# Kernel optimization log

Hardware: AMD Instinct MI355X
Metric: run time of the kernel (lower is better)

## Reference

```python
import jax, jax.numpy as jnp
import numpy as np

B, P, M, N, H, K, EH = 16, 50, 512, 1024, 64, 20, 200


def setup_inputs() -> dict:
    key = jax.random.key(0)
    ks = jax.random.split(key, 16)
    b = jax.random.normal(ks[0], (B, P, M, 1), jnp.float32)
    A = jax.random.normal(ks[1], (1, P, M, N), jnp.float32) / np.float32(np.sqrt(M))
    # random undirected multigraph on P nodes, stored with both directions
    s = jax.random.randint(ks[2], (B, EH), 0, P)
    off = jax.random.randint(ks[3], (B, EH), 1, P)
    d = (s + off) % P
    edge_index = jnp.stack([jnp.concatenate([s, d], 1), jnp.concatenate([d, s], 1)], 1).astype(jnp.int32)  # [B,2,2*EH]

    def lin(k, fi, fo, scale=None):
        scale = np.float32(1.0 / np.sqrt(fi)) if scale is None else np.float32(scale)
        return jax.random.normal(k, (fi, fo), jnp.float32) * scale, jnp.zeros((fo,), jnp.float32)

    W_e1, b_e1 = lin(ks[4], P * M, P * H)
    W_e2, b_e2 = lin(ks[5], P * H, 2 * P * H)
    W_e3, b_e3 = lin(ks[6], 2 * P * H, 4 * P * H)
    W_c1, b_c1 = lin(ks[7], 4 * H, 2 * H)
    W_c2, b_c2 = lin(ks[8], 2 * H, 2 * H)
    W_f1, b_f1 = lin(ks[9], 2 * H, H)
    W_f2, _ = lin(ks[10], H, K * 4, scale=1e-3)
    b_f2 = jnp.full((K * 4,), -2.0, jnp.float32)  # mimics fc2 init (tiny weights, negative bias)
    max_param = jnp.array([0.01, 0.1, 0.1, 0.1], jnp.float32).reshape(1, 1, 1, 4)  # [alpha,tau,rho,eta]_max
    y0 = jax.random.normal(ks[11], (B, P, N, 1), jnp.float32) * 0.01
    u0 = jax.random.normal(ks[12], (B, P, N, 1), jnp.float32) * 0.01
    d0 = jax.random.normal(ks[13], (B, P, N, 1), jnp.float32) * 0.01
    return dict(b=b, A=A, edge_index=edge_index, max_param=max_param,
                W_e1=W_e1, b_e1=b_e1, W_e2=W_e2, b_e2=b_e2, W_e3=W_e3, b_e3=b_e3,
                W_c1=W_c1, b_c1=b_c1, W_c2=W_c2, b_c2=b_c2,
                W_f1=W_f1, b_f1=b_f1, W_f2=W_f2, b_f2=b_f2,
                y0=y0, u0=u0, d0=d0)


def _lrelu(x):
    return jax.nn.leaky_relu(x, 0.01)


def _gcn(x, s, d, W, bias):
    # GCNConv: sym-normalized propagation with self loops. x: [P,F]
    h = x @ W
    deg = jnp.zeros((x.shape[0],), x.dtype).at[d].add(1.0) + 1.0  # +1 self loop
    dinv = jax.lax.rsqrt(deg)
    agg = jnp.zeros_like(h).at[d].add(h[s] * (dinv[s] * dinv[d])[:, None])
    agg = agg + h * (dinv * dinv)[:, None]  # self-loop term
    return agg + bias


def _delta(y, s, d):
    # nested neighbor loop: for each directed edge (s,d): delta[s]+=y[s]-y[d]; delta[d]-=same
    diff = y[s] - y[d]  # [E,N,1]
    return jnp.zeros_like(y).at[s].add(diff).at[d].add(-diff)


def reference(b, A, edge_index, max_param,
              W_e1, b_e1, W_e2, b_e2, W_e3, b_e3,
              W_c1, b_c1, W_c2, b_c2, W_f1, b_f1, W_f2, b_f2,
              y0, u0, d0):
    Bb = b.shape[0]
    n = A.shape[3]
    k_steps = W_f2.shape[1] // 4
    src, dst = edge_index[:, 0], edge_index[:, 1]

    # ---- GNN hypernetwork ----
    x = b.reshape(Bb, -1)
    x = _lrelu(x @ W_e1 + b_e1)
    x = _lrelu(x @ W_e2 + b_e2)
    x = (x @ W_e3 + b_e3).reshape(Bb, P, -1)  # [B,P,4H]
    x = _lrelu(jax.vmap(lambda xf, s, d: _gcn(xf, s, d, W_c1, b_c1))(x, src, dst))
    x = _lrelu(jax.vmap(lambda xf, s, d: _gcn(xf, s, d, W_c2, b_c2))(x, src, dst))
    x = x.mean(axis=1)  # global_mean_pool over nodes
    x = _lrelu(x @ W_f1 + b_f1)
    hyp = (x @ W_f2 + b_f2).reshape(Bb, k_steps, 1, 4)
    hyp = jax.nn.sigmoid(jnp.cumsum(hyp, axis=1)) * max_param  # [B,K,1,4]
    hyp_scan = jnp.transpose(hyp, (1, 3, 0, 2))[..., None, None]  # [K,4,B,1,1,1]

    # ---- precompute ----
    A0 = A[0]  # [P,M,N]
    AtA = jnp.einsum('pmn,pmk->pnk', A0, A0)  # [P,N,N]
    Atb = jnp.einsum('pmn,bpmo->bpno', A0, b)  # [B,P,N,1]
    sum_nb = jax.vmap(lambda s: jnp.zeros((P,), b.dtype).at[s].add(1.0))(src)[:, :, None, None]  # [B,P,1,1]

    # ---- unrolled D-ADMM / DLASSO ----
    def step(carry, hk):
        y_k, U_k, dlt = carry
        alpha, tau, rho, eta = hk[0], hk[1], hk[2], hk[3]
        AtAy = jnp.einsum('pnk,bpko->bpno', AtA, y_k)
        g = AtAy - Atb + jnp.sign(y_k) * tau + U_k * sum_nb + dlt * rho
        y_n = y_k - alpha * g
        dlt_n = jax.vmap(_delta)(y_n, src, dst)
        U_n = U_k + dlt_n * eta
        return (y_n, U_n, dlt_n), y_n

    _, Y = jax.lax.scan(step, (y0, u0, d0), hyp_scan)
    return Y  # [K,B,P,N,1]
```

## Files before the change

### kernel.cpp

```cpp
#include <hip/hip_runtime.h>

namespace {
constexpr int NB = 16;
constexpr int NP = 50;
constexpr int NM = 512;
constexpr int NN = 1024;
constexpr int NK = 20;
constexpr long ASZ = (long)NP * NM * NN;
constexpr long YSZ = (long)NB * NP * NN;
}

typedef __attribute__((ext_vector_type(8))) short bf16x8;
typedef __attribute__((ext_vector_type(4))) float f32x4;

__device__ __forceinline__ float lrelu(float x){ return x > 0.f ? x : 0.01f*x; }
__device__ __forceinline__ float bfu(unsigned short x){
  unsigned v = ((unsigned)x) << 16;
  return __builtin_bit_cast(float, v);
}
__device__ __forceinline__ unsigned short f2bf(float f){
  unsigned u = __builtin_bit_cast(unsigned, f);
  u += 0x7fffu + ((u >> 16) & 1u);
  return (unsigned short)(u >> 16);
}
__device__ __forceinline__ long toff(int n, int kk){
  return (long)(n>>4)*16384 + (long)(kk>>5)*512 + (long)((n&15)*32 + ((kk>>3)&3)*8 + (kk&7));
}

__global__ __launch_bounds__(256) void k_prep(const float* __restrict__ A,
                      unsigned short* __restrict__ abfT){
  const int p = blockIdx.x, mt = blockIdx.y, nt = blockIdx.z;
  const int tid = threadIdx.x;
  __shared__ unsigned short tile[64][72];
  const int m0 = mt*64, n0 = nt*64;
  {
    int r = tid>>2, cs = (tid&3)*16;
    const float* src = A + ((long)p*NM + m0 + r)*NN + n0 + cs;
    unsigned short tmp[16];
    #pragma unroll
    for (int q=0;q<16;q+=4){
      float4 v = *(const float4*)(src+q);
      tmp[q+0]=f2bf(v.x); tmp[q+1]=f2bf(v.y); tmp[q+2]=f2bf(v.z); tmp[q+3]=f2bf(v.w);
    }
    #pragma unroll
    for (int q=0;q<16;q++) tile[r][cs+q] = tmp[q];
  }
  __syncthreads();
  {
    int r = tid>>2, cs = (tid&3)*16;
    unsigned short* dst = abfT + ((long)p*NN + n0 + r)*NM + m0 + cs;
    unsigned short tmp[16];
    #pragma unroll
    for (int q=0;q<16;q++) tmp[q] = tile[cs+q][r];
    #pragma unroll
    for (int q=0;q<16;q+=8) *(uint4*)(dst+q) = *(const uint4*)&tmp[q];
  }
}

__global__ void k_init(const float* __restrict__ y0, float* __restrict__ y,
                       unsigned short* __restrict__ ybf, int n){
  int e = (blockIdx.x*blockDim.x + threadIdx.x)*4;
  if (e >= n) return;
  float4 a = *(const float4*)(y0+e);
  *(float4*)(y+e) = a;
  ushort4 o; o.x=f2bf(a.x); o.y=f2bf(a.y); o.z=f2bf(a.z); o.w=f2bf(a.w);
  *(ushort4*)(ybf+e) = o;
}

__global__ __launch_bounds__(256) void k_e0(const float* __restrict__ u0,
      const float* __restrict__ d0, const float* __restrict__ atb,
      const float* __restrict__ snbg, const float* __restrict__ hypg,
      float* __restrict__ w, float* __restrict__ e){
  long i = ((long)blockIdx.x*256 + threadIdx.x)*4;
  if (i >= YSZ) return;
  long bp = i >> 10;
  int b = (int)(bp/NP), p = (int)(bp%NP);
  float sp = snbg[b*NP+p], rho = hypg[b*80 + 2];
  float4 uv = *(const float4*)(u0+i);
  float4 dv = *(const float4*)(d0+i);
  float4 av = *(const float4*)(atb+i);
  float4 wv, ev;
  wv.x = uv.x*sp - av.x; wv.y = uv.y*sp - av.y;
  wv.z = uv.z*sp - av.z; wv.w = uv.w*sp - av.w;
  ev.x = wv.x + dv.x*rho; ev.y = wv.y + dv.y*rho;
  ev.z = wv.z + dv.z*rho; ev.w = wv.w + dv.w*rho;
  *(float4*)(w+i) = wv;
  *(float4*)(e+i) = ev;
}


__device__ __forceinline__ void enc_body(const float* __restrict__ X, const float* __restrict__ W,
                           float* __restrict__ part, int fi, int fo, int ichunk, int actin,
                           int bx, int c, int tid, char* smem){
  float (*xs)[16] = (float(*)[16])smem;
  const int o0 = (bx*256 + tid)*4;
  const bool ok = o0 < fo;
  float4 acc[16];
  #pragma unroll
  for (int b=0;b<16;b++){ acc[b].x=0.f; acc[b].y=0.f; acc[b].z=0.f; acc[b].w=0.f; }
  const long ibase = (long)c*ichunk;
  const int xb = tid&15, xio = (tid>>4)*4;
  for (int s=0; s<ichunk; s+=64){
    float4 v = *(const float4*)(X + (long)xb*fi + ibase + s + xio);
    if (actin){ v.x=lrelu(v.x); v.y=lrelu(v.y); v.z=lrelu(v.z); v.w=lrelu(v.w); }
    __syncthreads();
    xs[xio+0][xb]=v.x; xs[xio+1][xb]=v.y; xs[xio+2][xb]=v.z; xs[xio+3][xb]=v.w;
    __syncthreads();
    const float* wp = W + (ibase+s)*fo + o0;
    #pragma unroll 4
    for (int i=0;i<64;i++){
      float4 w;
      if (ok) w = *(const float4*)(wp + (long)i*fo);
      else { w.x=0.f; w.y=0.f; w.z=0.f; w.w=0.f; }
      #pragma unroll
      for (int b2=0;b2<16;b2+=4){
        float4 x4 = *(const float4*)&xs[i][b2];
        acc[b2+0].x += w.x*x4.x; acc[b2+0].y += w.y*x4.x; acc[b2+0].z += w.z*x4.x; acc[b2+0].w += w.w*x4.x;
        acc[b2+1].x += w.x*x4.y; acc[b2+1].y += w.y*x4.y; acc[b2+1].z += w.z*x4.y; acc[b2+1].w += w.w*x4.y;
        acc[b2+2].x += w.x*x4.z; acc[b2+2].y += w.y*x4.z; acc[b2+2].z += w.z*x4.z; acc[b2+2].w += w.w*x4.z;
        acc[b2+3].x += w.x*x4.w; acc[b2+3].y += w.y*x4.w; acc[b2+3].z += w.z*x4.w; acc[b2+3].w += w.w*x4.w;
      }
    }
  }
  if (ok){
    float* pp = part + ((long)c*16)*fo + o0;
    #pragma unroll
    for (int b=0;b<16;b++) *(float4*)(pp + (long)b*fo) = acc[b];
  }
}

__device__ __forceinline__ void ata_body(const unsigned short* __restrict__ abfT,
                      unsigned short* __restrict__ ata, int yy_in, int p, int tid, char* smem){
  unsigned short (*pa)[72] = (unsigned short(*)[72])smem;
  unsigned short (*pb)[72] = (unsigned short(*)[72])(smem + 18432);
  int yy = yy_in, bi = 0;
  while (yy >= 8 - bi){ yy -= 8 - bi; bi++; }
  const int bj = bi + yy;
  const int i0 = bi*128, j0 = bj*128;
  const int wave = tid>>6, lane = tid&63;
  const int lr = lane&15, kg = lane>>4;
  f32x4 acc[2][8];
  #pragma unroll
  for (int ti=0;ti<2;ti++)
    #pragma unroll
    for (int tj=0;tj<8;tj++) acc[ti][tj] = (f32x4){0.f,0.f,0.f,0.f};
  const unsigned short* Abase = abfT + (long)p*NN*NM;
  for (int mc=0; mc<NM; mc+=64){
    __syncthreads();
    {
      int r = tid>>1, c0 = (tid&1)*32;
      const unsigned short* sa = Abase + (long)(i0 + r)*NM + mc + c0;
      const unsigned short* sb = Abase + (long)(j0 + r)*NM + mc + c0;
      #pragma unroll
      for (int q=0;q<32;q+=8){
        *(uint4*)&pa[r][c0+q] = *(const uint4*)(sa+q);
        *(uint4*)&pb[r][c0+q] = *(const uint4*)(sb+q);
      }
    }
    __syncthreads();
    #pragma unroll
    for (int ks=0; ks<2; ks++){
      bf16x8 av0 = *(const bf16x8*)&pa[wave*32      + lr][ks*32 + kg*8];
      bf16x8 av1 = *(const bf16x8*)&pa[wave*32 + 16 + lr][ks*32 + kg*8];
      #pragma unroll
      for (int tj=0;tj<8;tj++){
        bf16x8 bv = *(const bf16x8*)&pb[tj*16 + lr][ks*32 + kg*8];
        acc[0][tj] = __builtin_amdgcn_mfma_f32_16x16x32_bf16(av0, bv, acc[0][tj], 0,0,0);
        acc[1][tj] = __builtin_amdgcn_mfma_f32_16x16x32_bf16(av1, bv, acc[1][tj], 0,0,0);
      }
    }
  }
  const long pbase = (long)p << 20;
  #pragma unroll
  for (int ti=0; ti<2; ti++){
    const int ib = i0 + wave*32 + ti*16;
    #pragma unroll
    for (int tj=0; tj<8; tj++){
      const int jb = j0 + tj*16;
      unsigned short w[4];
      #pragma unroll
      for (int r=0;r<4;r++) w[r] = f2bf(acc[ti][tj][r]);
      #pragma unroll
      for (int r=0;r<4;r++)
        ata[pbase + toff(ib + kg*4 + r, jb + lr)] = w[r];
      if (bi != bj){
        #pragma unroll
        for (int r=0;r<4;r++)
          ata[pbase + toff(jb + lr, ib + kg*4 + r)] = w[r];
      }
    }
  }
}

__device__ __forceinline__ void atb_body(const unsigned short* __restrict__ abfT,
                      const float* __restrict__ src, float* __restrict__ z,
                      int p, int gy, int tid, char* smem){
  unsigned short (*tlds)[520] = (unsigned short(*)[520])smem;
  const int wave = tid>>6, lane = tid&63;
  {
    int b = tid>>4, c0 = (tid&15)*8;
    const float* tr = src + ((long)b*NP + p)*NM;
    #pragma unroll
    for (int it=0; it<4; it++){
      float4 lo = *(const float4*)(tr + it*128 + c0);
      float4 hi = *(const float4*)(tr + it*128 + c0 + 4);
      unsigned short w[8];
      w[0]=f2bf(lo.x); w[1]=f2bf(lo.y); w[2]=f2bf(lo.z); w[3]=f2bf(lo.w);
      w[4]=f2bf(hi.x); w[5]=f2bf(hi.y); w[6]=f2bf(hi.z); w[7]=f2bf(hi.w);
      *(uint4*)&tlds[b][it*128 + c0] = *(const uint4*)w;
    }
  }
  __syncthreads();
  const int lr = lane&15, kg = lane>>4;
  const int nt0 = gy*4 + wave;
  const int n0 = nt0*16, n1 = (nt0+32)*16;
  const unsigned short* b0 = abfT + ((long)p*NN + n0 + lr)*NM + kg*8;
  const unsigned short* b1 = abfT + ((long)p*NN + n1 + lr)*NM + kg*8;
  const unsigned short* tp = &tlds[lr][kg*8];
  f32x4 acc0a={0.f,0.f,0.f,0.f}, acc0b={0.f,0.f,0.f,0.f};
  f32x4 acc1a={0.f,0.f,0.f,0.f}, acc1b={0.f,0.f,0.f,0.f};
  #pragma unroll 4
  for (int ks=0; ks<16; ks+=2){
    bf16x8 t0 = *(const bf16x8*)(tp + ks*32);
    bf16x8 t1 = *(const bf16x8*)(tp + ks*32 + 32);
    bf16x8 b00 = *(const bf16x8*)(b0 + (long)ks*32);
    bf16x8 b01 = *(const bf16x8*)(b0 + (long)ks*32 + 32);
    bf16x8 b10 = *(const bf16x8*)(b1 + (long)ks*32);
    bf16x8 b11 = *(const bf16x8*)(b1 + (long)ks*32 + 32);
    acc0a = __builtin_amdgcn_mfma_f32_16x16x32_bf16(t0, b00, acc0a, 0, 0, 0);
    acc1a = __builtin_amdgcn_mfma_f32_16x16x32_bf16(t0, b10, acc1a, 0, 0, 0);
    acc0b = __builtin_amdgcn_mfma_f32_16x16x32_bf16(t1, b01, acc0b, 0, 0, 0);
    acc1b = __builtin_amdgcn_mfma_f32_16x16x32_bf16(t1, b11, acc1b, 0, 0, 0);
  }
  f32x4 acc0 = acc0a + acc0b;
  f32x4 acc1 = acc1a + acc1b;
  #pragma unroll
  for (int r=0;r<4;r++){
    int bb = kg*4 + r;
    z[((long)bb*NP + p)*NN + n0 + lr] = acc0[r];
    z[((long)bb*NP + p)*NN + n1 + lr] = acc1[r];
  }
}

__global__ __launch_bounds__(256) void k_big(const unsigned short* __restrict__ abfT,
      unsigned short* __restrict__ ata, const float* __restrict__ bin,
      const float* __restrict__ We1, float* __restrict__ part,
      float* __restrict__ atb){
  __shared__ __align__(16) char smem[36864];
  const int bid = blockIdx.x, tid = threadIdx.x;
  if (bid < 800){
    enc_body(bin, We1, part, 25600, 3200, 128, 0, bid & 3, bid >> 2, tid, smem);
  } else if (bid < 2600){
    int a = bid - 800;
    ata_body(abfT, ata, a % 36, a / 36, tid, smem);
  } else {
    int a = bid - 2600;
    atb_body(abfT, bin, atb, a >> 3, a & 7, tid, smem);
  }
}

__global__ __launch_bounds__(256) void k_enc2(const float* __restrict__ X, const float* __restrict__ W,
                           float* __restrict__ part, int fi, int fo, int ichunk, int actin){
  __shared__ __align__(16) char smem[4096];
  enc_body(X, W, part, fi, fo, ichunk, actin, blockIdx.x, blockIdx.y, threadIdx.x, smem);
}

__global__ void k_enc_reduce(const float* __restrict__ part, const float* __restrict__ bias,
                             float* __restrict__ out, int fo, int nchunk){
  int i = blockIdx.x*256 + threadIdx.x;
  if (i >= 16*fo) return;
  int o = i % fo;
  float s = bias[o];
  for (int c=0;c<nchunk;c++) s += part[(long)c*16*fo + i];
  out[i] = s;
}

__global__ __launch_bounds__(64) void k_graph(const int* __restrict__ ei, float* __restrict__ adjg,
                        float* __restrict__ dmg, float* __restrict__ snbg){
  const int b = blockIdx.x, tid = threadIdx.x;
  __shared__ float adj[2500], dm[2500], deg[50], dinv[50], snb[50];
  for (int i=tid;i<2500;i+=64){ adj[i]=0.f; dm[i]=0.f; }
  if (tid<50){ deg[tid]=0.f; snb[tid]=0.f; }
  __syncthreads();
  const int* e = ei + b*800;
  for (int k=tid;k<400;k+=64){
    atomicAdd(&deg[e[400+k]], 1.f);
    atomicAdd(&snb[e[k]], 1.f);
  }
  __syncthreads();
  if (tid<50) dinv[tid] = 1.f / sqrtf(deg[tid] + 1.f);
  __syncthreads();
  for (int k=tid;k<400;k+=64){
    int s = e[k], d = e[400+k];
    atomicAdd(&adj[d*50+s], dinv[s]*dinv[d]);
    atomicAdd(&dm[s*50+s],  1.f); atomicAdd(&dm[s*50+d], -1.f);
    atomicAdd(&dm[d*50+d],  1.f); atomicAdd(&dm[d*50+s], -1.f);
  }
  __syncthreads();
  if (tid<50) adj[tid*50+tid] += dinv[tid]*dinv[tid];
  __syncthreads();
  for (int i=tid;i<2500;i+=64){ adjg[b*2500+i]=adj[i]; dmg[b*2500+i]=dm[i]; }
  if (tid<50) snbg[b*50+tid]=snb[tid];
}

__global__ __launch_bounds__(256) void k_gnn(const float* __restrict__ h3,
     const float* __restrict__ Wc1, const float* __restrict__ bc1,
     const float* __restrict__ Wc2, const float* __restrict__ bc2,
     const float* __restrict__ Wf1, const float* __restrict__ bf1,
     const float* __restrict__ Wf2, const float* __restrict__ bf2,
     const float* __restrict__ maxp, const float* __restrict__ adjg,
     float* __restrict__ hypg){
  const int b = blockIdx.x, tid = threadIdx.x;
  __shared__ float adj[2500];
  __shared__ float bufA[6400];
  __shared__ float bufB[6400];
  __shared__ float xm[128], hv1[64], raw[80];
  for (int i=tid;i<2500;i+=256) adj[i] = adjg[b*2500+i];

  const int j = tid & 127, nh = tid >> 7;
  float acc[25];
  #pragma unroll
  for (int q=0;q<25;q++) acc[q]=0.f;
  for (int ic=0; ic<4; ic++){
    __syncthreads();
    for (int e=tid; e<800; e+=256){
      int n = e>>4, seg = (e&15)*4;
      *(float4*)&bufB[n*64+seg] = *(const float4*)(h3 + (long)b*12800 + n*256 + ic*64 + seg);
    }
    __syncthreads();
    for (int i=0;i<64;i+=4){
      float w0 = Wc1[(long)(ic*64+i+0)*128 + j];
      float w1 = Wc1[(long)(ic*64+i+1)*128 + j];
      float w2 = Wc1[(long)(ic*64+i+2)*128 + j];
      float w3 = Wc1[(long)(ic*64+i+3)*128 + j];
      #pragma unroll
      for (int q=0;q<25;q++){
        float4 xv = *(const float4*)&bufB[(nh*25+q)*64 + i];
        acc[q] += xv.x*w0 + xv.y*w1 + xv.z*w2 + xv.w*w3;
      }
    }
  }
  __syncthreads();
  #pragma unroll
  for (int q=0;q<25;q++) bufA[(nh*25+q)*128 + j] = acc[q];
  __syncthreads();
  {
    float a2[25];
    float bv = bc1[j];
    #pragma unroll
    for (int q=0;q<25;q++) a2[q]=bv;
    for (int qq=0; qq<50; qq++){
      float hvv = bufA[qq*128 + j];
      #pragma unroll
      for (int q=0;q<25;q++) a2[q] += adj[(nh*25+q)*50 + qq]*hvv;
    }
    __syncthreads();
    #pragma unroll
    for (int q=0;q<25;q++) bufB[(nh*25+q)*128 + j] = lrelu(a2[q]);
  }
  __syncthreads();
  {
    float a2[25];
    #pragma unroll
    for (int q=0;q<25;q++) a2[q]=0.f;
    for (int i=0;i<128;i+=4){
      float w0 = Wc2[(long)(i+0)*128 + j];
      float w1 = Wc2[(long)(i+1)*128 + j];
      float w2 = Wc2[(long)(i+2)*128 + j];
      float w3 = Wc2[(long)(i+3)*128 + j];
      #pragma unroll
      for (int q=0;q<25;q++){
        float4 xv = *(const float4*)&bufB[(nh*25+q)*128 + i];
        a2[q] += xv.x*w0 + xv.y*w1 + xv.z*w2 + xv.w*w3;
      }
    }
    __syncthreads();
    #pragma unroll
    for (int q=0;q<25;q++) bufA[(nh*25+q)*128 + j] = a2[q];
  }
  __syncthreads();
  {
    float a2[25];
    float bv = bc2[j];
    #pragma unroll
    for (int q=0;q<25;q++) a2[q]=bv;
    for (int qq=0; qq<50; qq++){
      float hvv = bufA[qq*128 + j];
      #pragma unroll
      for (int q=0;q<25;q++) a2[q] += adj[(nh*25+q)*50 + qq]*hvv;
    }
    __syncthreads();
    #pragma unroll
    for (int q=0;q<25;q++) bufB[(nh*25+q)*128 + j] = lrelu(a2[q]);
  }
  __syncthreads();
  if (tid < 128){
    float s = 0.f;
    for (int n=0;n<50;n++) s += bufB[n*128 + tid];
    xm[tid] = s * (1.f/50.f);
  }
  __syncthreads();
  if (tid < 64){
    float s = bf1[tid];
    for (int i=0;i<128;i++) s += xm[i]*Wf1[i*64 + tid];
    hv1[tid] = lrelu(s);
  }
  __syncthreads();
  if (tid < 80){
    float s = bf2[tid];
    for (int i=0;i<64;i++) s += hv1[i]*Wf2[i*80 + tid];
    raw[tid] = s;
  }
  __syncthreads();
  if (tid < 4){
    float c = 0.f;
    for (int k=0;k<20;k++){
      c += raw[k*4 + tid];
      hypg[b*80 + k*4 + tid] = maxp[tid] / (1.f + expf(-c));
    }
  }
}

__global__ __launch_bounds__(256, 4) void k_z(const unsigned short* __restrict__ ata,
      const unsigned short* __restrict__ ybin, const float* __restrict__ ebuf,
      const float* __restrict__ hypg, int k,
      float* __restrict__ y, unsigned short* __restrict__ ybout,
      float* __restrict__ yout){
  const int p = blockIdx.x;
  const int tid = threadIdx.x, wave = tid>>6, lane = tid&63;
  __shared__ unsigned short ylds[16][1032];
  {
    int b = tid>>4, c0 = (tid&15)*8;
    const unsigned short* yr = ybin + ((long)b*NP + p)*NN;
    #pragma unroll
    for (int it=0; it<8; it++)
      *(uint4*)&ylds[b][it*128 + c0] = *(const uint4*)(yr + it*128 + c0);
  }
  const int lr = lane&15, kg = lane>>4;
  const int t  = blockIdx.y*4 + wave;
  const int n0 = t*16;
  const unsigned short* bp = ata + ((long)p<<20) + (long)t*16384 + lr*32 + kg*8;
  const unsigned short* yp = &ylds[lr][kg*8];

  bf16x8 B[3][4];
  #pragma unroll
  for (int j=0;j<4;j++) B[0][j] = *(const bf16x8*)(bp + (0*4+j)*512);
  #pragma unroll
  for (int j=0;j<4;j++) B[1][j] = *(const bf16x8*)(bp + (1*4+j)*512);

  float yv4[4], e4[4];
  float4 hp4[4];
  #pragma unroll
  for (int r=0;r<4;r++){
    const int b = kg*4 + r;
    const long idx = ((long)b*NP + p)*NN + n0 + lr;
    yv4[r] = y[idx]; e4[r] = ebuf[idx];
    hp4[r] = *(const float4*)(hypg + b*80 + k*4);
  }
  __syncthreads();

  f32x4 a0={0.f,0.f,0.f,0.f}, a1={0.f,0.f,0.f,0.f}, a2={0.f,0.f,0.f,0.f}, a3={0.f,0.f,0.f,0.f};
  #pragma unroll
  for (int i=0;i<8;i++){
    const int cur = i % 3;
    const int nxt = (i+2) % 3;
    if (i < 6){
      #pragma unroll
      for (int j=0;j<4;j++) B[nxt][j] = *(const bf16x8*)(bp + ((i+2)*4+j)*512);
    }
    bf16x8 q0 = *(const bf16x8*)(yp + (i*4+0)*32);
    bf16x8 q1 = *(const bf16x8*)(yp + (i*4+1)*32);
    bf16x8 q2 = *(const bf16x8*)(yp + (i*4+2)*32);
    bf16x8 q3 = *(const bf16x8*)(yp + (i*4+3)*32);
    a0 = __builtin_amdgcn_mfma_f32_16x16x32_bf16(q0, B[cur][0], a0, 0,0,0);
    a1 = __builtin_amdgcn_mfma_f32_16x16x32_bf16(q1, B[cur][1], a1, 0,0,0);
    a2 = __builtin_amdgcn_mfma_f32_16x16x32_bf16(q2, B[cur][2], a2, 0,0,0);
    a3 = __builtin_amdgcn_mfma_f32_16x16x32_bf16(q3, B[cur][3], a3, 0,0,0);
  }
  f32x4 z = (a0 + a1) + (a2 + a3);
  #pragma unroll
  for (int r=0;r<4;r++){
    const int b = kg*4 + r;
    const long idx = ((long)b*NP + p)*NN + n0 + lr;
    float yv = yv4[r];
    float g = z[r] + ((yv>0.f)?1.f:((yv<0.f)?-1.f:0.f))*hp4[r].y + e4[r];
    float ynv = yv - hp4[r].x*g;
    y[idx] = ynv; ybout[idx] = f2bf(ynv); yout[(long)k*YSZ + idx] = ynv;
  }
}

__global__ __launch_bounds__(256) void k_dm(const float* __restrict__ dmg,
      const float* __restrict__ snbg, const float* __restrict__ hypg, int k,
      const unsigned short* __restrict__ ybf, float* __restrict__ w, float* __restrict__ e){
  const int b = blockIdx.x, n0 = blockIdx.y*64, tid = threadIdx.x;
  __shared__ float ys[50][64];
  __shared__ float dms[2500];
  for (int i=tid;i<2500;i+=256) dms[i] = dmg[b*2500+i];
  for (int i=tid; i<3200; i+=256){
    int p=i>>6, nn=i&63;
    ys[p][nn] = bfu(ybf[((long)b*NP+p)*NN + n0 + nn]);
  }
  __syncthreads();
  const float eta = hypg[b*80 + k*4 + 3];
  const float rhon = hypg[b*80 + (k+1)*4 + 2];
  for (int i=tid; i<3200; i+=256){
    int p=i>>6, nn=i&63;
    float s=0.f;
    #pragma unroll 10
    for (int q=0;q<NP;q++) s += dms[p*50+q]*ys[q][nn];
    long idx = ((long)b*NP+p)*NN + n0 + nn;
    float wn = w[idx] + s*eta*snbg[b*NP+p];
    w[idx] = wn;
    e[idx] = wn + s*rhon;
  }
}

extern "C" void kernel_launch(void* const* d_in, const int* in_sizes, int n_in,
                              void* d_out, int out_size, void* d_ws, size_t ws_size,
                              hipStream_t stream){
  (void)in_sizes; (void)n_in; (void)out_size; (void)ws_size;
  const float* bin = (const float*)d_in[0];
  const float* A   = (const float*)d_in[1];
  const int*   ei  = (const int*)d_in[2];
  const float* mxp = (const float*)d_in[3];
  const float* We1 = (const float*)d_in[4];  const float* be1 = (const float*)d_in[5];
  const float* We2 = (const float*)d_in[6];  const float* be2 = (const float*)d_in[7];
  const float* We3 = (const float*)d_in[8];  const float* be3 = (const float*)d_in[9];
  const float* Wc1 = (const float*)d_in[10]; const float* bc1 = (const float*)d_in[11];
  const float* Wc2 = (const float*)d_in[12]; const float* bc2 = (const float*)d_in[13];
  const float* Wf1 = (const float*)d_in[14]; const float* bf1 = (const float*)d_in[15];
  const float* Wf2 = (const float*)d_in[16]; const float* bf2 = (const float*)d_in[17];
  const float* y0  = (const float*)d_in[18];
  const float* u0  = (const float*)d_in[19];
  const float* dd0 = (const float*)d_in[20];
  float* out = (float*)d_out;

  char* cur = (char*)d_ws;
  auto alloc = [&](size_t bytes)->void*{
    void* pp = (void*)cur; cur += (bytes + 255) & ~(size_t)255; return pp;
  };
  unsigned short* abfT = (unsigned short*)alloc(ASZ*2);
  unsigned short* ata  = (unsigned short*)alloc((size_t)NP*1024*1024*2);
  float* atb = (float*)alloc(YSZ*4);
  float* y   = (float*)alloc(YSZ*4);
  unsigned short* ybf0 = (unsigned short*)alloc(YSZ*2);
  unsigned short* ybf1 = (unsigned short*)alloc(YSZ*2);
  float* w   = (float*)alloc(YSZ*4);
  float* eb  = (float*)alloc(YSZ*4);
  float* h1  = (float*)alloc((size_t)16*3200*4);
  float* h2  = (float*)alloc((size_t)16*6400*4);
  float* h3  = (float*)alloc((size_t)16*12800*4);
  float* adj = (float*)alloc((size_t)16*2500*4);
  float* dm  = (float*)alloc((size_t)16*2500*4);
  float* snb = (float*)alloc((size_t)16*50*4);
  float* hyp = (float*)alloc((size_t)16*80*4);
  float* part= (float*)alloc((size_t)84000000);

  k_prep<<<dim3(50,8,16), dim3(256), 0, stream>>>(A, abfT);
  k_init<<<dim3(800), dim3(256), 0, stream>>>(y0, y, ybf0, (int)YSZ);

  k_big<<<dim3(3000), dim3(256), 0, stream>>>(abfT, ata, bin, We1, part, atb);
  k_enc_reduce<<<dim3(200), dim3(256), 0, stream>>>(part, be1, h1, 3200, 200);

  k_enc2<<<dim3(7,100),  dim3(256), 0, stream>>>(h1, We2, part, 3200, 6400, 32, 1);
  k_enc_reduce<<<dim3(400), dim3(256), 0, stream>>>(part, be2, h2, 6400, 100);
  k_enc2<<<dim3(13,100), dim3(256), 0, stream>>>(h2, We3, part, 6400, 12800, 64, 1);
  k_enc_reduce<<<dim3(800), dim3(256), 0, stream>>>(part, be3, h3, 12800, 100);

  k_graph<<<dim3(16), dim3(64), 0, stream>>>(ei, adj, dm, snb);
  k_gnn<<<dim3(16), dim3(256), 0, stream>>>(h3, Wc1, bc1, Wc2, bc2, Wf1, bf1, Wf2, bf2, mxp, adj, hyp);
  k_e0<<<dim3(800), dim3(256), 0, stream>>>(u0, dd0, atb, snb, hyp, w, eb);

  for (int k=0;k<NK;k++){
    const unsigned short* ybin = (k & 1) ? ybf1 : ybf0;
    unsigned short* ybout      = (k & 1) ? ybf0 : ybf1;
    k_z<<<dim3(50,16), dim3(256), 0, stream>>>(ata, ybin, eb, hyp, k, y, ybout, out);
    if (k < NK-1){
      const unsigned short* ybnew = (k & 1) ? ybf0 : ybf1;
      k_dm<<<dim3(16,16), dim3(256), 0, stream>>>(dm, snb, hyp, k, ybnew, w, eb);
    }
  }
}
```

Baseline: 1.359 ms.

## Fold graph build into k_big, widen encoder chunks, drop LDS staging in k_z

Moves the per-batch graph construction into k_big as extra blocks, which removes one launch. The first encoder layer now uses 256-row input chunks, so it needs half as many blocks and reduction partials. k_z no longer stages y in LDS or software-pipelines the AtA loads: each wave reads y and AtA fragments directly from global memory, and the launch-bounds occupancy hint rises from 4 to 6. This gets rid of the LDS fill and barrier but leaves load latency hidden only by occupancy, and y is re-read redundantly by each wave.

New measurement: 1.382 ms. About the same (+1.6%).

```diff
diff --git a/kernel.cpp b/kernel.cpp
--- a/kernel.cpp
+++ b/kernel.cpp
@@ -242,20 +242,54 @@
   }
 }
 
+__device__ __forceinline__ void graph_body(const int* __restrict__ ei, float* __restrict__ adjg,
+                      float* __restrict__ dmg, float* __restrict__ snbg, int b, int tid, char* smem){
+  float* adj = (float*)smem;
+  float* dm  = adj + 2500;
+  float* deg = dm + 2500;
+  float* dinv= deg + 50;
+  float* snb = dinv + 50;
+  for (int i=tid;i<2500;i+=256){ adj[i]=0.f; dm[i]=0.f; }
+  if (tid<50){ deg[tid]=0.f; snb[tid]=0.f; }
+  __syncthreads();
+  const int* e = ei + b*800;
+  for (int k=tid;k<400;k+=256){
+    atomicAdd(&deg[e[400+k]], 1.f);
+    atomicAdd(&snb[e[k]], 1.f);
+  }
+  __syncthreads();
+  if (tid<50) dinv[tid] = 1.f / sqrtf(deg[tid] + 1.f);
+  __syncthreads();
+  for (int k=tid;k<400;k+=256){
+    int s = e[k], d = e[400+k];
+    atomicAdd(&adj[d*50+s], dinv[s]*dinv[d]);
+    atomicAdd(&dm[s*50+s],  1.f); atomicAdd(&dm[s*50+d], -1.f);
+    atomicAdd(&dm[d*50+d],  1.f); atomicAdd(&dm[d*50+s], -1.f);
+  }
+  __syncthreads();
+  if (tid<50) adj[tid*50+tid] += dinv[tid]*dinv[tid];
+  __syncthreads();
+  for (int i=tid;i<2500;i+=256){ adjg[b*2500+i]=adj[i]; dmg[b*2500+i]=dm[i]; }
+  if (tid<50) snbg[b*50+tid]=snb[tid];
+}
+
 __global__ __launch_bounds__(256) void k_big(const unsigned short* __restrict__ abfT,
       unsigned short* __restrict__ ata, const float* __restrict__ bin,
       const float* __restrict__ We1, float* __restrict__ part,
-      float* __restrict__ atb){
+      float* __restrict__ atb, const int* __restrict__ ei,
+      float* __restrict__ adjg, float* __restrict__ dmg, float* __restrict__ snbg){
   __shared__ __align__(16) char smem[36864];
   const int bid = blockIdx.x, tid = threadIdx.x;
-  if (bid < 800){
-    enc_body(bin, We1, part, 25600, 3200, 128, 0, bid & 3, bid >> 2, tid, smem);
+  if (bid < 400){
+    enc_body(bin, We1, part, 25600, 3200, 256, 0, bid & 3, bid >> 2, tid, smem);
+  } else if (bid < 2200){
+    int a = bid - 400;
+    ata_body(abfT, ata, a % 36, a / 36, tid, smem);
   } else if (bid < 2600){
-    int a = bid - 800;
-    ata_body(abfT, ata, a % 36, a / 36, tid, smem);
+    int a = bid - 2200;
+    atb_body(abfT, bin, atb, a >> 3, a & 7, tid, smem);
   } else {
-    int a = bid - 2600;
-    atb_body(abfT, bin, atb, a >> 3, a & 7, tid, smem);
+    graph_body(ei, adjg, dmg, snbg, bid - 2600, tid, smem);
   }
 }
 
@@ -273,34 +307,6 @@
   float s = bias[o];
   for (int c=0;c<nchunk;c++) s += part[(long)c*16*fo + i];
   out[i] = s;
-}
-
-__global__ __launch_bounds__(64) void k_graph(const int* __restrict__ ei, float* __restrict__ adjg,
-                        float* __restrict__ dmg, float* __restrict__ snbg){
-  const int b = blockIdx.x, tid = threadIdx.x;
-  __shared__ float adj[2500], dm[2500], deg[50], dinv[50], snb[50];
-  for (int i=tid;i<2500;i+=64){ adj[i]=0.f; dm[i]=0.f; }
-  if (tid<50){ deg[tid]=0.f; snb[tid]=0.f; }
-  __syncthreads();
-  const int* e = ei + b*800;
-  for (int k=tid;k<400;k+=64){
-    atomicAdd(&deg[e[400+k]], 1.f);
-    atomicAdd(&snb[e[k]], 1.f);
-  }
-  __syncthreads();
-  if (tid<50) dinv[tid] = 1.f / sqrtf(deg[tid] + 1.f);
-  __syncthreads();
-  for (int k=tid;k<400;k+=64){
-    int s = e[k], d = e[400+k];
-    atomicAdd(&adj[d*50+s], dinv[s]*dinv[d]);
-    atomicAdd(&dm[s*50+s],  1.f); atomicAdd(&dm[s*50+d], -1.f);
-    atomicAdd(&dm[d*50+d],  1.f); atomicAdd(&dm[d*50+s], -1.f);
-  }
-  __syncthreads();
-  if (tid<50) adj[tid*50+tid] += dinv[tid]*dinv[tid];
-  __syncthreads();
-  for (int i=tid;i<2500;i+=64){ adjg[b*2500+i]=adj[i]; dmg[b*2500+i]=dm[i]; }
-  if (tid<50) snbg[b*50+tid]=snb[tid];
 }
 
 __global__ __launch_bounds__(256) void k_gnn(const float* __restrict__ h3,
@@ -421,32 +427,18 @@
   }
 }
 
-__global__ __launch_bounds__(256, 4) void k_z(const unsigned short* __restrict__ ata,
+__global__ __launch_bounds__(256, 6) void k_z(const unsigned short* __restrict__ ata,
       const unsigned short* __restrict__ ybin, const float* __restrict__ ebuf,
       const float* __restrict__ hypg, int k,
       float* __restrict__ y, unsigned short* __restrict__ ybout,
       float* __restrict__ yout){
   const int p = blockIdx.x;
   const int tid = threadIdx.x, wave = tid>>6, lane = tid&63;
-  __shared__ unsigned short ylds[16][1032];
-  {
-    int b = tid>>4, c0 = (tid&15)*8;
-    const unsigned short* yr = ybin + ((long)b*NP + p)*NN;
-    #pragma unroll
-    for (int it=0; it<8; it++)
-      *(uint4*)&ylds[b][it*128 + c0] = *(const uint4*)(yr + it*128 + c0);
-  }
   const int lr = lane&15, kg = lane>>4;
   const int t  = blockIdx.y*4 + wave;
   const int n0 = t*16;
-  const unsigned short* bp = ata + ((long)p<<20) + (long)t*16384 + lr*32 + kg*8;
-  const unsigned short* yp = &ylds[lr][kg*8];
-
-  bf16x8 B[3][4];
-  #pragma unroll
-  for (int j=0;j<4;j++) B[0][j] = *(const bf16x8*)(bp + (0*4+j)*512);
-  #pragma unroll
-  for (int j=0;j<4;j++) B[1][j] = *(const bf16x8*)(bp + (1*4+j)*512);
+  const unsigned short* bp  = ata + ((long)p<<20) + (long)t*16384 + lr*32 + kg*8;
+  const unsigned short* ypg = ybin + ((long)lr*NP + p)*NN + kg*8;
 
   float yv4[4], e4[4];
   float4 hp4[4];
@@ -457,25 +449,22 @@
     yv4[r] = y[idx]; e4[r] = ebuf[idx];
     hp4[r] = *(const float4*)(hypg + b*80 + k*4);
   }
-  __syncthreads();
 
   f32x4 a0={0.f,0.f,0.f,0.f}, a1={0.f,0.f,0.f,0.f}, a2={0.f,0.f,0.f,0.f}, a3={0.f,0.f,0.f,0.f};
   #pragma unroll
   for (int i=0;i<8;i++){
-    const int cur = i % 3;
-    const int nxt = (i+2) % 3;
-    if (i < 6){
-      #pragma unroll
-      for (int j=0;j<4;j++) B[nxt][j] = *(const bf16x8*)(bp + ((i+2)*4+j)*512);
-    }
-    bf16x8 q0 = *(const bf16x8*)(yp + (i*4+0)*32);
-    bf16x8 q1 = *(const bf16x8*)(yp + (i*4+1)*32);
-    bf16x8 q2 = *(const bf16x8*)(yp + (i*4+2)*32);
-    bf16x8 q3 = *(const bf16x8*)(yp + (i*4+3)*32);
-    a0 = __builtin_amdgcn_mfma_f32_16x16x32_bf16(q0, B[cur][0], a0, 0,0,0);
-    a1 = __builtin_amdgcn_mfma_f32_16x16x32_bf16(q1, B[cur][1], a1, 0,0,0);
-    a2 = __builtin_amdgcn_mfma_f32_16x16x32_bf16(q2, B[cur][2], a2, 0,0,0);
-    a3 = __builtin_amdgcn_mfma_f32_16x16x32_bf16(q3, B[cur][3], a3, 0,0,0);
+    bf16x8 b0 = *(const bf16x8*)(bp + (i*4+0)*512);
+    bf16x8 b1 = *(const bf16x8*)(bp + (i*4+1)*512);
+    bf16x8 b2 = *(const bf16x8*)(bp + (i*4+2)*512);
+    bf16x8 b3 = *(const bf16x8*)(bp + (i*4+3)*512);
+    bf16x8 q0 = *(const bf16x8*)(ypg + (i*4+0)*32);
+    bf16x8 q1 = *(const bf16x8*)(ypg + (i*4+1)*32);
+    bf16x8 q2 = *(const bf16x8*)(ypg + (i*4+2)*32);
+    bf16x8 q3 = *(const bf16x8*)(ypg + (i*4+3)*32);
+    a0 = __builtin_amdgcn_mfma_f32_16x16x32_bf16(q0, b0, a0, 0,0,0);
+    a1 = __builtin_amdgcn_mfma_f32_16x16x32_bf16(q1, b1, a1, 0,0,0);
+    a2 = __builtin_amdgcn_mfma_f32_16x16x32_bf16(q2, b2, a2, 0,0,0);
+    a3 = __builtin_amdgcn_mfma_f32_16x16x32_bf16(q3, b3, a3, 0,0,0);
   }
   f32x4 z = (a0 + a1) + (a2 + a3);
   #pragma unroll
@@ -559,15 +548,15 @@
   k_prep<<<dim3(50,8,16), dim3(256), 0, stream>>>(A, abfT);
   k_init<<<dim3(800), dim3(256), 0, stream>>>(y0, y, ybf0, (int)YSZ);
 
-  k_big<<<dim3(3000), dim3(256), 0, stream>>>(abfT, ata, bin, We1, part, atb);
-  k_enc_reduce<<<dim3(200), dim3(256), 0, stream>>>(part, be1, h1, 3200, 200);
+  k_big<<<dim3(2616), dim3(256), 0, stream>>>(abfT, ata, bin, We1, part, atb,
+                                              ei, adj, dm, snb);
+  k_enc_reduce<<<dim3(200), dim3(256), 0, stream>>>(part, be1, h1, 3200, 100);
 
   k_enc2<<<dim3(7,100),  dim3(256), 0, stream>>>(h1, We2, part, 3200, 6400, 32, 1);
   k_enc_reduce<<<dim3(400), dim3(256), 0, stream>>>(part, be2, h2, 6400, 100);
   k_enc2<<<dim3(13,100), dim3(256), 0, stream>>>(h2, We3, part, 6400, 12800, 64, 1);
   k_enc_reduce<<<dim3(800), dim3(256), 0, stream>>>(part, be3, h3, 12800, 100);
 
-  k_graph<<<dim3(16), dim3(64), 0, stream>>>(ei, adj, dm, snb);
   k_gnn<<<dim3(16), dim3(256), 0, stream>>>(h3, Wc1, bc1, Wc2, bc2, Wf1, bf1, Wf2, bf2, mxp, adj, hyp);
   k_e0<<<dim3(800), dim3(256), 0, stream>>>(u0, dd0, atb, snb, hyp, w, eb);
 
```
